# Kernel optimization log

Hardware: AMD Instinct MI355X
Metric: run time of the kernel (lower is better)

## Reference

```python
import jax, jax.numpy as jnp
import numpy as np

D_MODEL = 256; N_HEADS = 8; HEAD_DIM = 32; N_LEVELS = 4; N_POINTS = 4; N_LAYERS = 3; D_FFN = 1024
SHAPES = np.array([[76, 76], [38, 38], [19, 19], [10, 10]], dtype=np.int64)
S_TOTAL = int((SHAPES[:, 0] * SHAPES[:, 1]).sum())  # 7681


def setup_inputs():
    key = jax.random.key(0)
    ks = jax.random.split(key, 12)
    B = 1; C = D_MODEL; M = N_HEADS; Lv = N_LEVELS; P = N_POINTS; L = N_LAYERS; s = 0.02
    starts = np.concatenate([[0], np.cumsum(SHAPES[:, 0] * SHAPES[:, 1])[:-1]]).astype(np.int64)
    inp = {
        "src": jax.random.normal(ks[0], (B, S_TOTAL, C), jnp.float32),
        "pos": jax.random.normal(ks[1], (B, S_TOTAL, C), jnp.float32),
        "valid_ratios": jnp.ones((B, Lv, 2), jnp.float32),
        "spatial_shapes": jnp.asarray(SHAPES),
        "level_start_index": jnp.asarray(starts),
        "padding_mask": jnp.zeros((B, S_TOTAL), bool),
        "W_off": jax.random.normal(ks[2], (L, C, M * Lv * P * 2), jnp.float32) * s,
        "b_off": jax.random.normal(ks[3], (L, M * Lv * P * 2), jnp.float32) * s,
        "W_attn": jax.random.normal(ks[4], (L, C, M * Lv * P), jnp.float32) * s,
        "b_attn": jax.random.normal(ks[5], (L, M * Lv * P), jnp.float32) * s,
        "W_val": jax.random.normal(ks[6], (L, C, C), jnp.float32) * s,
        "b_val": jnp.zeros((L, C), jnp.float32),
        "W_out": jax.random.normal(ks[7], (L, C, C), jnp.float32) * s,
        "b_out": jnp.zeros((L, C), jnp.float32),
        "ln1_g": jnp.ones((L, C), jnp.float32),
        "ln1_b": jnp.zeros((L, C), jnp.float32),
        "W_ff1": jax.random.normal(ks[8], (L, C, D_FFN), jnp.float32) * s,
        "b_ff1": jnp.zeros((L, D_FFN), jnp.float32),
        "W_ff2": jax.random.normal(ks[9], (L, D_FFN, C), jnp.float32) * s,
        "b_ff2": jnp.zeros((L, C), jnp.float32),
        "ln2_g": jnp.ones((L, C), jnp.float32),
        "ln2_b": jnp.zeros((L, C), jnp.float32),
    }
    return inp


def _ln(x, g, b):
    mu = x.mean(-1, keepdims=True)
    var = ((x - mu) ** 2).mean(-1, keepdims=True)
    return (x - mu) * jax.lax.rsqrt(var + 1e-5) * g + b


def _gather(v, idx):
    # v: [B, HW, M, D], idx: [B, S, M, P] -> [B, S, M, P, D], head-specific gather
    B, S, M, P = idx.shape
    def one(vb, ib):
        i2 = ib.transpose(0, 2, 1).reshape(S * P, M, 1)
        o = jnp.take_along_axis(vb, i2, axis=0)  # [S*P, M, D]
        return o.reshape(S, P, M, -1).transpose(0, 2, 1, 3)
    return jax.vmap(one)(v, idx)


def _msda(query, src, mask, ref, shapes, starts, Wo, bo, Wa, ba, Wv, bv, Wout, bout):
    # Multi-scale deformable attention (Deformable-DETR), grid_sample align_corners=False + zero padding
    B, S, C = src.shape
    M, Lv, P, D = N_HEADS, N_LEVELS, N_POINTS, HEAD_DIM
    value = src @ Wv + bv
    value = jnp.where(mask[..., None], 0.0, value).reshape(B, S, M, D)
    off = (query @ Wo + bo).reshape(B, S, M, Lv, P, 2)
    aw = jax.nn.softmax((query @ Wa + ba).reshape(B, S, M, Lv * P), -1).reshape(B, S, M, Lv, P)
    norm = jnp.asarray(shapes[:, ::-1].copy(), jnp.float32)  # (W, H) per level
    loc = ref[:, :, None, :, None, :] + off / norm[None, None, None, :, None, :]  # [B,S,M,Lv,P,2]
    out = jnp.zeros((B, S, M, D), query.dtype)
    for lvl in range(Lv):
        H = int(shapes[lvl, 0]); W = int(shapes[lvl, 1]); st = int(starts[lvl])
        v = value[:, st:st + H * W]  # [B, H*W, M, D]
        l = loc[:, :, :, lvl]  # [B, S, M, P, 2]
        x = l[..., 0] * W - 0.5
        y = l[..., 1] * H - 0.5
        x0 = jnp.floor(x); y0 = jnp.floor(y)
        dx = x - x0; dy = y - y0
        samp = jnp.zeros((B, S, M, P, D), query.dtype)
        for yy, xx, w in ((y0, x0, (1 - dy) * (1 - dx)), (y0, x0 + 1, (1 - dy) * dx),
                          (y0 + 1, x0, dy * (1 - dx)), (y0 + 1, x0 + 1, dy * dx)):
            valid = (xx >= 0) & (xx < W) & (yy >= 0) & (yy < H)
            xi = jnp.clip(xx, 0, W - 1).astype(jnp.int32)
            yi = jnp.clip(yy, 0, H - 1).astype(jnp.int32)
            g = _gather(v, yi * W + xi)
            samp = samp + (w * valid)[..., None] * g
        out = out + (aw[:, :, :, lvl, :, None] * samp).sum(3)
    return out.reshape(B, S, C) @ Wout + bout


def _ref_points(vr, shapes):
    refs = []
    for lvl in range(shapes.shape[0]):
        H = int(shapes[lvl, 0]); W = int(shapes[lvl, 1])
        ry, rx = np.meshgrid(np.linspace(0.5, H - 0.5, H, dtype=np.float32),
                             np.linspace(0.5, W - 0.5, W, dtype=np.float32), indexing="ij")
        rxj = jnp.asarray(rx.reshape(-1))[None] / (vr[:, None, lvl, 0] * W)
        ryj = jnp.asarray(ry.reshape(-1))[None] / (vr[:, None, lvl, 1] * H)
        refs.append(jnp.stack([rxj, ryj], -1))
    ref = jnp.concatenate(refs, 1)  # [B, S, 2]
    return ref[:, :, None] * vr[:, None]  # [B, S, Lv, 2]


def _encoder(src, pos, valid_ratios, shapes, starts, mask, params):
    (W_off, b_off, W_attn, b_attn, W_val, b_val, W_out, b_out,
     ln1_g, ln1_b, W_ff1, b_ff1, W_ff2, b_ff2, ln2_g, ln2_b) = params
    ref = _ref_points(valid_ratios, shapes)
    out = src
    for l in range(N_LAYERS):
        q = out + pos  # with_pos_embed
        a = _msda(q, out, mask, ref, shapes, starts, W_off[l], b_off[l], W_attn[l], b_attn[l],
                  W_val[l], b_val[l], W_out[l], b_out[l])
        out = _ln(out + a, ln1_g[l], ln1_b[l])
        f = jax.nn.relu(out @ W_ff1[l] + b_ff1[l]) @ W_ff2[l] + b_ff2[l]
        out = _ln(out + f, ln2_g[l], ln2_b[l])
    return out


def reference(src, pos, valid_ratios, spatial_shapes, level_start_index, padding_mask,
              W_off, b_off, W_attn, b_attn, W_val, b_val, W_out, b_out,
              ln1_g, ln1_b, W_ff1, b_ff1, W_ff2, b_ff2, ln2_g, ln2_b):
    shapes = np.asarray(spatial_shapes)
    starts = np.asarray(level_start_index)
    params = (W_off, b_off, W_attn, b_attn, W_val, b_val, W_out, b_out,
              ln1_g, ln1_b, W_ff1, b_ff1, W_ff2, b_ff2, ln2_g, ln2_b)
    return _encoder(src, pos, valid_ratios, shapes, starts, padding_mask, params)
```

## Files before the change

### kernel.cpp

```cpp
#include <hip/hip_runtime.h>
#include <hip/hip_bf16.h>
#include <math.h>

#define S_TOTAL 7681

typedef __attribute__((ext_vector_type(8))) short bf16x8;
typedef __attribute__((ext_vector_type(4))) float f32x4;

__device__ __forceinline__ short f2b(float x) {
    union { float f; unsigned u; } v; v.f = x;
    unsigned r = v.u + 0x7FFFu + ((v.u >> 16) & 1u);
    return (short)(r >> 16);
}
__device__ __forceinline__ float b2f(unsigned short u) {
    union { unsigned u; float f; } t; t.u = ((unsigned)u) << 16; return t.f;
}

__device__ __forceinline__ void gll16(const short* g, short* l) {
    __builtin_amdgcn_global_load_lds(
        (const __attribute__((address_space(1))) unsigned int*)g,
        (__attribute__((address_space(3))) unsigned int*)l,
        16, 0, 0);
}

#define MFMA16(a, b, c) __builtin_amdgcn_mfma_f32_16x16x32_bf16(a, b, c, 0, 0, 0)

__global__ __launch_bounds__(256) void transpose_cvt_kernel(
    const float* __restrict__ s0, const float* __restrict__ s1,
    const float* __restrict__ s2, const float* __restrict__ s3,
    const float* __restrict__ s4, const float* __restrict__ s5,
    short* __restrict__ d0, short* __restrict__ d1, short* __restrict__ d2,
    short* __restrict__ d3, short* __restrict__ d4, short* __restrict__ d5)
{
    const int z = blockIdx.z;
    int t = blockIdx.x;
    const float* src; short* dst; int K, N, lt;
    if (t < 64)       { src = s0 + (size_t)z * 65536;  dst = d0 + (size_t)z * 65536;  K = 256;  N = 256;  lt = t; }
    else if (t < 128) { src = s1 + (size_t)z * 65536;  dst = d1 + (size_t)z * 98304;  K = 256;  N = 256;  lt = t - 64; }
    else if (t < 160) { src = s2 + (size_t)z * 32768;  dst = d2 + (size_t)z * 98304;  K = 256;  N = 128;  lt = t - 128; }
    else if (t < 224) { src = s3 + (size_t)z * 65536;  dst = d3 + (size_t)z * 65536;  K = 256;  N = 256;  lt = t - 160; }
    else if (t < 480) { src = s4 + (size_t)z * 262144; dst = d4 + (size_t)z * 262144; K = 256;  N = 1024; lt = t - 224; }
    else              { src = s5 + (size_t)z * 262144; dst = d5 + (size_t)z * 262144; K = 1024; N = 256;  lt = t - 480; }
    const int ntx = N >> 5;
    const int tk = (lt / ntx) << 5, tn = (lt % ntx) << 5;
    __shared__ float tile[32][33];
    const int cx = threadIdx.x & 31, cy = threadIdx.x >> 5;
    #pragma unroll
    for (int i = 0; i < 32; i += 8)
        tile[cy + i][cx] = src[(size_t)(tk + cy + i) * N + tn + cx];
    __syncthreads();
    #pragma unroll
    for (int i = 0; i < 32; i += 8)
        dst[(size_t)(tn + cy + i) * K + tk + cx] = f2b(tile[cx][cy + i]);
}

__global__ __launch_bounds__(256) void gemm_va_kernel(
    const short* __restrict__ xb, const short* __restrict__ qb,
    const short* __restrict__ Wt_val, const short* __restrict__ Wt_oa,
    const float* __restrict__ b_val, const float* __restrict__ b_off,
    const float* __restrict__ b_attn,
    short* __restrict__ value_bf, float* __restrict__ offbuf, int M)
{
    const int grp = (blockIdx.y >= 4);
    const short* A  = grp ? qb : xb;
    const short* Wt = grp ? Wt_oa : Wt_val;
    const int colBase = (grp ? (blockIdx.y - 4) : blockIdx.y) * 64;
    const int K = 256;

    __shared__ __align__(16) short As[2][128 * 32];
    __shared__ __align__(16) short Bs[2][64 * 32];

    const int tid = threadIdx.x;
    const int lane = tid & 63;
    const int wave = tid >> 6;
    const int rowBase = blockIdx.x * 128;

    const int sr  = lane >> 2;
    const int skp = (lane & 3) * 8;
    const short* gA0 = A + (size_t)min(rowBase + wave * 16 + sr, M - 1) * K + skp;
    const short* gA1 = A + (size_t)min(rowBase + 64 + wave * 16 + sr, M - 1) * K + skp;
    const short* gB  = Wt + (size_t)(colBase + wave * 16 + sr) * K + skp;

    const int frow = lane & 15;
    const int fko  = (lane >> 4) * 8;
    const int wm = wave * 32;

    f32x4 acc[2][4] = {};

    gll16(gA0, &As[0][wave * 512]);
    gll16(gA1, &As[0][2048 + wave * 512]);
    gll16(gB,  &Bs[0][wave * 512]);
    __syncthreads();

    int cur = 0;
    for (int k0 = 0; k0 < K; k0 += 32) {
        const int nxt = cur ^ 1;
        if (k0 + 32 < K) {
            gll16(gA0 + k0 + 32, &As[nxt][wave * 512]);
            gll16(gA1 + k0 + 32, &As[nxt][2048 + wave * 512]);
            gll16(gB  + k0 + 32, &Bs[nxt][wave * 512]);
        }
        bf16x8 af0 = *(const bf16x8*)&As[cur][(wm + frow) * 32 + fko];
        bf16x8 af1 = *(const bf16x8*)&As[cur][(wm + 16 + frow) * 32 + fko];
        #pragma unroll
        for (int j = 0; j < 4; ++j) {
            bf16x8 bfj = *(const bf16x8*)&Bs[cur][(j * 16 + frow) * 32 + fko];
            acc[0][j] = MFMA16(af0, bfj, acc[0][j]);
            acc[1][j] = MFMA16(af1, bfj, acc[1][j]);
        }
        __syncthreads();
        cur = nxt;
    }

    const int erow = (lane >> 4) * 4;
    const int ecol = lane & 15;
    #pragma unroll
    for (int mi = 0; mi < 2; ++mi) {
        #pragma unroll
        for (int j = 0; j < 4; ++j) {
            int col = colBase + j * 16 + ecol;
            float bias = grp ? (col < 256 ? b_off[col] : b_attn[col - 256]) : b_val[col];
            #pragma unroll
            for (int r = 0; r < 4; ++r) {
                int row = rowBase + wm + mi * 16 + erow + r;
                if (row < M) {
                    float v = acc[mi][j][r] + bias;
                    if (grp) offbuf[(size_t)row * 384 + col] = v;
                    else     value_bf[(size_t)row * 256 + col] = f2b(v);
                }
            }
        }
    }
}

template<int RELU, int OUTBF>
__global__ __launch_bounds__(256) void gemm_kernel(
    const short* __restrict__ A, const short* __restrict__ Wt,
    const float* __restrict__ bias, void* __restrict__ Cv,
    int M, int N, int K)
{
    __shared__ __align__(16) short As[2][128 * 32];
    __shared__ __align__(16) short Bs[2][64 * 32];

    const int tid = threadIdx.x;
    const int lane = tid & 63;
    const int wave = tid >> 6;
    const int rowBase = blockIdx.x * 128;
    const int colBase = blockIdx.y * 64;

    const int sr  = lane >> 2;
    const int skp = (lane & 3) * 8;
    const short* gA0 = A + (size_t)min(rowBase + wave * 16 + sr, M - 1) * K + skp;
    const short* gA1 = A + (size_t)min(rowBase + 64 + wave * 16 + sr, M - 1) * K + skp;
    const short* gB  = Wt + (size_t)(colBase + wave * 16 + sr) * K + skp;

    const int frow = lane & 15;
    const int fko  = (lane >> 4) * 8;
    const int wm = wave * 32;

    f32x4 acc[2][4] = {};

    gll16(gA0, &As[0][wave * 512]);
    gll16(gA1, &As[0][2048 + wave * 512]);
    gll16(gB,  &Bs[0][wave * 512]);
    __syncthreads();

    int cur = 0;
    for (int k0 = 0; k0 < K; k0 += 32) {
        const int nxt = cur ^ 1;
        if (k0 + 32 < K) {
            gll16(gA0 + k0 + 32, &As[nxt][wave * 512]);
            gll16(gA1 + k0 + 32, &As[nxt][2048 + wave * 512]);
            gll16(gB  + k0 + 32, &Bs[nxt][wave * 512]);
        }
        bf16x8 af0 = *(const bf16x8*)&As[cur][(wm + frow) * 32 + fko];
        bf16x8 af1 = *(const bf16x8*)&As[cur][(wm + 16 + frow) * 32 + fko];
        #pragma unroll
        for (int j = 0; j < 4; ++j) {
            bf16x8 bfj = *(const bf16x8*)&Bs[cur][(j * 16 + frow) * 32 + fko];
            acc[0][j] = MFMA16(af0, bfj, acc[0][j]);
            acc[1][j] = MFMA16(af1, bfj, acc[1][j]);
        }
        __syncthreads();
        cur = nxt;
    }

    const int erow = (lane >> 4) * 4;
    const int ecol = lane & 15;
    #pragma unroll
    for (int mi = 0; mi < 2; ++mi) {
        #pragma unroll
        for (int j = 0; j < 4; ++j) {
            #pragma unroll
            for (int r = 0; r < 4; ++r) {
                int row = rowBase + wm + mi * 16 + erow + r;
                if (row < M) {
                    int col = colBase + j * 16 + ecol;
                    float v = acc[mi][j][r] + bias[col];
                    if (RELU) v = fmaxf(v, 0.f);
                    if (OUTBF) ((short*)Cv)[(size_t)row * N + col] = f2b(v);
                    else       ((float*)Cv)[(size_t)row * N + col] = v;
                }
            }
        }
    }
}

template<int WRITEQ>
__global__ __launch_bounds__(256) void gemm_ln_kernel(
    const short* __restrict__ A, const short* __restrict__ Wt,
    const float* __restrict__ bias, const float* __restrict__ g,
    const float* __restrict__ bln, const float* __restrict__ pos,
    float* __restrict__ out, short* __restrict__ xb, short* __restrict__ qb,
    int M, int K)
{
    __shared__ __align__(16) short As[2][16 * 32];
    __shared__ __align__(16) short Bs[2][256 * 32];
    __shared__ float rsum[16][4], rsq[16][4], smu[16], srs[16];

    const int tid = threadIdx.x;
    const int lane = tid & 63;
    const int wave = tid >> 6;
    const int rowBase = blockIdx.x * 16;

    const int sr  = lane >> 2;
    const int skp = (lane & 3) * 8;
    const short* gA = A + (size_t)min(rowBase + sr, M - 1) * K + skp;
    const short* gB = Wt + (size_t)(wave * 16 + sr) * K + skp;

    const int frow = lane & 15;
    const int fko  = (lane >> 4) * 8;

    f32x4 acc[4] = {};

    if (wave == 0) gll16(gA, &As[0][0]);
    gll16(gB,                       &Bs[0][wave * 512]);
    gll16(gB + (size_t)64  * K,     &Bs[0][2048 + wave * 512]);
    gll16(gB + (size_t)128 * K,     &Bs[0][4096 + wave * 512]);
    gll16(gB + (size_t)192 * K,     &Bs[0][6144 + wave * 512]);
    __syncthreads();

    int cur = 0;
    for (int k0 = 0; k0 < K; k0 += 32) {
        const int nxt = cur ^ 1;
        if (k0 + 32 < K) {
            const int kn = k0 + 32;
            if (wave == 0) gll16(gA + kn, &As[nxt][0]);
            gll16(gB + kn,                   &Bs[nxt][wave * 512]);
            gll16(gB + (size_t)64  * K + kn, &Bs[nxt][2048 + wave * 512]);
            gll16(gB + (size_t)128 * K + kn, &Bs[nxt][4096 + wave * 512]);
            gll16(gB + (size_t)192 * K + kn, &Bs[nxt][6144 + wave * 512]);
        }
        bf16x8 af = *(const bf16x8*)&As[cur][frow * 32 + fko];
        #pragma unroll
        for (int j = 0; j < 4; ++j) {
            bf16x8 bfj = *(const bf16x8*)&Bs[cur][(wave * 64 + j * 16 + frow) * 32 + fko];
            acc[j] = MFMA16(af, bfj, acc[j]);
        }
        __syncthreads();
        cur = nxt;
    }

    const int erow = (lane >> 4) * 4;
    const int ecol = lane & 15;
    float x[4][4];
    #pragma unroll
    for (int j = 0; j < 4; ++j)
        #pragma unroll
        for (int r = 0; r < 4; ++r) {
            int row = rowBase + erow + r;
            int col = wave * 64 + j * 16 + ecol;
            float res = (row < M) ? out[(size_t)row * 256 + col] : 0.f;
            x[j][r] = acc[j][r] + bias[col] + res;
        }

    #pragma unroll
    for (int r = 0; r < 4; ++r) {
        float s1 = x[0][r] + x[1][r] + x[2][r] + x[3][r];
        float s2 = x[0][r]*x[0][r] + x[1][r]*x[1][r]
                 + x[2][r]*x[2][r] + x[3][r]*x[3][r];
        #pragma unroll
        for (int o = 1; o < 16; o <<= 1) {
            s1 += __shfl_xor(s1, o);
            s2 += __shfl_xor(s2, o);
        }
        if ((lane & 15) == 0) {
            rsum[erow + r][wave] = s1;
            rsq [erow + r][wave] = s2;
        }
    }
    __syncthreads();
    if (tid < 16) {
        float S1 = rsum[tid][0] + rsum[tid][1] + rsum[tid][2] + rsum[tid][3];
        float S2 = rsq[tid][0] + rsq[tid][1] + rsq[tid][2] + rsq[tid][3];
        float mu = S1 * (1.f / 256.f);
        smu[tid] = mu;
        srs[tid] = rsqrtf(S2 * (1.f / 256.f) - mu * mu + 1e-5f);
    }
    __syncthreads();

    #pragma unroll
    for (int r = 0; r < 4; ++r) {
        int lrow = erow + r;
        int row = rowBase + lrow;
        if (row >= M) continue;
        float mu = smu[lrow], rs = srs[lrow];
        #pragma unroll
        for (int j = 0; j < 4; ++j) {
            int col = wave * 64 + j * 16 + ecol;
            float y = (x[j][r] - mu) * rs * g[col] + bln[col];
            out[(size_t)row * 256 + col] = y;
            xb[(size_t)row * 256 + col] = f2b(y);
            if (WRITEQ)
                qb[(size_t)row * 256 + col] = f2b(y + pos[(size_t)row * 256 + col]);
        }
    }
}

__global__ __launch_bounds__(256) void msda_kernel(
    const short* __restrict__ value, const float* __restrict__ offb,
    short* __restrict__ msdab)
{
    __shared__ float   soff[8 * 384];
    __shared__ ushort4 sIdx[1024];
    __shared__ float4  sWgt[1024];

    const int bid = blockIdx.x;
    const int sb = (bid & 7) * 121 + (bid >> 3);
    const int q0 = sb * 8;
    if (q0 >= S_TOTAL) return;
    const int tid = threadIdx.x;

    {
        const float4* src4 = (const float4*)offb;
        #pragma unroll
        for (int i = tid; i < 768; i += 256) {
            int qi = i / 96, j = i - qi * 96;
            int q = min(q0 + qi, S_TOTAL - 1);
            *(float4*)&soff[qi * 384 + j * 4] = src4[(size_t)q * 96 + j];
        }
    }
    __syncthreads();

    if (tid < 64) {
        const int qi = tid >> 3, m = tid & 7;
        float* lg = &soff[qi * 384 + 256 + m * 16];
        float mx = -1e30f;
        #pragma unroll
        for (int k = 0; k < 16; ++k) mx = fmaxf(mx, lg[k]);
        float e[16], sum = 0.f;
        #pragma unroll
        for (int k = 0; k < 16; ++k) { e[k] = expf(lg[k] - mx); sum += e[k]; }
        float inv = 1.f / sum;
        #pragma unroll
        for (int k = 0; k < 16; ++k) lg[k] = e[k] * inv;
    }
    __syncthreads();

    #pragma unroll
    for (int it = tid; it < 1024; it += 256) {
        const int qi = it >> 7, i = it & 127;
        const int lvl = (i >> 2) & 3;
        const int q = min(q0 + qi, S_TOTAL - 1);

        float refx, refy;
        if (q < 5776)      { int t = q;        int r = t / 76, c = t % 76; refx = (c + 0.5f) / 76.f; refy = (r + 0.5f) / 76.f; }
        else if (q < 7220) { int t = q - 5776; int r = t / 38, c = t % 38; refx = (c + 0.5f) / 38.f; refy = (r + 0.5f) / 38.f; }
        else if (q < 7581) { int t = q - 7220; int r = t / 19, c = t % 19; refx = (c + 0.5f) / 19.f; refy = (r + 0.5f) / 19.f; }
        else               { int t = q - 7581; int r = t / 10, c = t % 10; refx = (c + 0.5f) / 10.f; refy = (r + 0.5f) / 10.f; }

        const int LVL_HW[4] = {76, 38, 19, 10};
        const int LVL_ST[4] = {0, 5776, 7220, 7581};
        const int W = LVL_HW[lvl];
        const float fW = (float)W;

        float ox = soff[qi * 384 + i * 2];
        float oy = soff[qi * 384 + i * 2 + 1];
        float aw = soff[qi * 384 + 256 + i];

        float x = refx * fW + ox - 0.5f;
        float y = refy * fW + oy - 0.5f;
        float x0f = floorf(x), y0f = floorf(y);
        int x0 = (int)x0f, y0 = (int)y0f;
        float dx = x - x0f, dy = y - y0f;

        bool vx0 = (x0 >= 0) & (x0 < W);
        bool vx1 = (x0 >= -1) & (x0 < W - 1);
        bool vy0 = (y0 >= 0) & (y0 < W);
        bool vy1 = (y0 >= -1) & (y0 < W - 1);
        int xc0 = min(max(x0, 0), W - 1), xc1 = min(max(x0 + 1, 0), W - 1);
        int yc0 = min(max(y0, 0), W - 1), yc1 = min(max(y0 + 1, 0), W - 1);
        int base = LVL_ST[lvl];
        ushort4 id;
        id.x = (unsigned short)(base + yc0 * W + xc0);
        id.y = (unsigned short)(base + yc0 * W + xc1);
        id.z = (unsigned short)(base + yc1 * W + xc0);
        id.w = (unsigned short)(base + yc1 * W + xc1);
        float4 w4;
        w4.x = (vy0 && vx0) ? (1.f - dy) * (1.f - dx) * aw : 0.f;
        w4.y = (vy0 && vx1) ? (1.f - dy) * dx * aw : 0.f;
        w4.z = (vy1 && vx0) ? dy * (1.f - dx) * aw : 0.f;
        w4.w = (vy1 && vx1) ? dy * dx * aw : 0.f;
        sIdx[it] = id;
        sWgt[it] = w4;
    }
    __syncthreads();

    const int lane = tid & 63;
    const int qi = (tid >> 6) * 2 + (lane >> 5);
    const int q = q0 + qi;
    if (q >= S_TOTAL) return;
    const int l32 = lane & 31;
    const int h = l32 >> 2, dg = l32 & 3;
    const short* vcol = value + h * 32 + dg * 8;
    const int itb = qi * 128 + (h << 4);

    float a[8] = {};
    #pragma unroll
    for (int pt = 0; pt < 16; ++pt) {
        const ushort4 id = sIdx[itb + pt];
        const float4 w = sWgt[itb + pt];
        bf16x8 v0 = *(const bf16x8*)(vcol + ((size_t)id.x << 8));
        bf16x8 v1 = *(const bf16x8*)(vcol + ((size_t)id.y << 8));
        bf16x8 v2 = *(const bf16x8*)(vcol + ((size_t)id.z << 8));
        bf16x8 v3 = *(const bf16x8*)(vcol + ((size_t)id.w << 8));
        #pragma unroll
        for (int e = 0; e < 8; ++e)
            a[e] += w.x * b2f((unsigned short)v0[e]) + w.y * b2f((unsigned short)v1[e])
                  + w.z * b2f((unsigned short)v2[e]) + w.w * b2f((unsigned short)v3[e]);
    }
    bf16x8 o;
    #pragma unroll
    for (int e = 0; e < 8; ++e) o[e] = f2b(a[e]);
    *(bf16x8*)(msdab + (size_t)q * 256 + h * 32 + dg * 8) = o;
}

__global__ __launch_bounds__(256) void cvt_copy_kernel(
    const float4* __restrict__ src, const float4* __restrict__ pos,
    float4* __restrict__ o, ushort4* __restrict__ xb, ushort4* __restrict__ qb,
    int n4)
{
    int i = blockIdx.x * blockDim.x + threadIdx.x;
    if (i < n4) {
        float4 v = src[i], p = pos[i];
        o[i] = v;
        ushort4 h, hq;
        h.x = (unsigned short)f2b(v.x); h.y = (unsigned short)f2b(v.y);
        h.z = (unsigned short)f2b(v.z); h.w = (unsigned short)f2b(v.w);
        hq.x = (unsigned short)f2b(v.x + p.x); hq.y = (unsigned short)f2b(v.y + p.y);
        hq.z = (unsigned short)f2b(v.z + p.z); hq.w = (unsigned short)f2b(v.w + p.w);
        xb[i] = h;
        qb[i] = hq;
    }
}

extern "C" void kernel_launch(void* const* d_in, const int* in_sizes, int n_in,
                              void* d_out, int out_size, void* d_ws, size_t ws_size,
                              hipStream_t stream) {
    const float* src    = (const float*)d_in[0];
    const float* pos    = (const float*)d_in[1];
    const float* W_off  = (const float*)d_in[6];
    const float* b_off  = (const float*)d_in[7];
    const float* W_attn = (const float*)d_in[8];
    const float* b_attn = (const float*)d_in[9];
    const float* W_val  = (const float*)d_in[10];
    const float* b_val  = (const float*)d_in[11];
    const float* W_out  = (const float*)d_in[12];
    const float* b_out  = (const float*)d_in[13];
    const float* ln1_g  = (const float*)d_in[14];
    const float* ln1_b  = (const float*)d_in[15];
    const float* W_ff1  = (const float*)d_in[16];
    const float* b_ff1  = (const float*)d_in[17];
    const float* W_ff2  = (const float*)d_in[18];
    const float* b_ff2  = (const float*)d_in[19];
    const float* ln2_g  = (const float*)d_in[20];
    const float* ln2_b  = (const float*)d_in[21];

    const size_t S = S_TOTAL;
    float* out = (float*)d_out;

    short* wt = (short*)d_ws;
    short* Wt_val = wt;
    short* Wt_oa  = wt + 196608;
    short* Wt_out = wt + 491520;
    short* Wt_ff1 = wt + 688128;
    short* Wt_ff2 = wt + 1474560;
    float* fbase  = (float*)d_ws + 1131648;
    short* xb       = (short*)fbase;
    short* qb       = (short*)(fbase + 128 * S);
    short* value_bf = (short*)(fbase + 256 * S);
    float* offb     = fbase + 384 * S;
    short* msdab    = (short*)(fbase + 768 * S);
    short* hid      = (short*)(fbase + 256 * S);

    transpose_cvt_kernel<<<dim3(736, 1, 3), 256, 0, stream>>>(
        W_val, W_off, W_attn, W_out, W_ff1, W_ff2,
        Wt_val, Wt_oa, Wt_oa + 65536, Wt_out, Wt_ff1, Wt_ff2);

    const int n4 = (int)(S * 256 / 4);
    const int g4 = (n4 + 255) / 256;
    cvt_copy_kernel<<<g4, 256, 0, stream>>>((const float4*)src, (const float4*)pos,
                                            (float4*)out, (ushort4*)xb, (ushort4*)qb, n4);

    const int MB = (S_TOTAL + 127) / 128;
    const int LB = (S_TOTAL + 15) / 16;

    for (int l = 0; l < 3; ++l) {
        gemm_va_kernel<<<dim3(MB, 10), 256, 0, stream>>>(
            xb, qb, Wt_val + (size_t)l * 65536, Wt_oa + (size_t)l * 98304,
            b_val + (size_t)l * 256, b_off + (size_t)l * 256, b_attn + (size_t)l * 128,
            value_bf, offb, S_TOTAL);
        msda_kernel<<<968, 256, 0, stream>>>(value_bf, offb, msdab);
        gemm_ln_kernel<0><<<LB, 256, 0, stream>>>(
            msdab, Wt_out + (size_t)l * 65536, b_out + (size_t)l * 256,
            ln1_g + (size_t)l * 256, ln1_b + (size_t)l * 256, pos,
            out, xb, qb, S_TOTAL, 256);
        gemm_kernel<1, 1><<<dim3(MB, 16), 256, 0, stream>>>(
            xb, Wt_ff1 + (size_t)l * 262144, b_ff1 + (size_t)l * 1024, hid,
            S_TOTAL, 1024, 256);
        gemm_ln_kernel<1><<<LB, 256, 0, stream>>>(
            hid, Wt_ff2 + (size_t)l * 262144, b_ff2 + (size_t)l * 256,
            ln2_g + (size_t)l * 256, ln2_b + (size_t)l * 256, pos,
            out, xb, qb, S_TOTAL, 1024);
    }
}
```

Measured before the change: 382.6 us.

## Use BK=64 with XOR-swizzled LDS tiles and fuse input conversion into weight transpose

All three bf16 GEMM kernels now stage a K-tile of 64 instead of 32, which halves the number of barrier rounds. The LDS layout is XOR-swizzled so the wider MFMA fragment reads avoid bank conflicts. The __syncthreads calls are replaced with explicit vmcnt waits plus raw s_barrier so the next tile's loads can stay in flight. Separately, the src/pos conversion kernel is merged into the weight-transpose kernel as extra blocks, removing one launch. The trade-offs are double the LDS per block, which can lower occupancy (notably in gemm_ln, with 256x64 B tiles), and hand-counted vmcnt values that must match the issued load count.

```diff
diff --git a/kernel.cpp b/kernel.cpp
--- a/kernel.cpp
+++ b/kernel.cpp
@@ -23,6 +23,8 @@
         16, 0, 0);
 }
 
+#define SBAR() asm volatile("s_barrier" ::: "memory")
+
 #define MFMA16(a, b, c) __builtin_amdgcn_mfma_f32_16x16x32_bf16(a, b, c, 0, 0, 0)
 
 __global__ __launch_bounds__(256) void transpose_cvt_kernel(
@@ -30,10 +32,28 @@
     const float* __restrict__ s2, const float* __restrict__ s3,
     const float* __restrict__ s4, const float* __restrict__ s5,
     short* __restrict__ d0, short* __restrict__ d1, short* __restrict__ d2,
-    short* __restrict__ d3, short* __restrict__ d4, short* __restrict__ d5)
+    short* __restrict__ d3, short* __restrict__ d4, short* __restrict__ d5,
+    const float4* __restrict__ csrc, const float4* __restrict__ cpos,
+    float4* __restrict__ co, ushort4* __restrict__ cxb, ushort4* __restrict__ cqb)
 {
     const int z = blockIdx.z;
     int t = blockIdx.x;
+    if (t >= 736) {
+        const int n4 = S_TOTAL * 64;
+        int i = (z * 641 + (t - 736)) * 256 + threadIdx.x;
+        if (i < n4) {
+            float4 v = csrc[i], p = cpos[i];
+            co[i] = v;
+            ushort4 h, hq;
+            h.x = (unsigned short)f2b(v.x); h.y = (unsigned short)f2b(v.y);
+            h.z = (unsigned short)f2b(v.z); h.w = (unsigned short)f2b(v.w);
+            hq.x = (unsigned short)f2b(v.x + p.x); hq.y = (unsigned short)f2b(v.y + p.y);
+            hq.z = (unsigned short)f2b(v.z + p.z); hq.w = (unsigned short)f2b(v.w + p.w);
+            cxb[i] = h;
+            cqb[i] = hq;
+        }
+        return;
+    }
     const float* src; short* dst; int K, N, lt;
     if (t < 64)       { src = s0 + (size_t)z * 65536;  dst = d0 + (size_t)z * 65536;  K = 256;  N = 256;  lt = t; }
     else if (t < 128) { src = s1 + (size_t)z * 65536;  dst = d1 + (size_t)z * 98304;  K = 256;  N = 256;  lt = t - 64; }
@@ -53,6 +73,7 @@
     for (int i = 0; i < 32; i += 8)
         dst[(size_t)(tn + cy + i) * K + tk + cx] = f2b(tile[cx][cy + i]);
 }
+
 
 __global__ __launch_bounds__(256) void gemm_va_kernel(
     const short* __restrict__ xb, const short* __restrict__ qb,
@@ -67,49 +88,67 @@
     const int colBase = (grp ? (blockIdx.y - 4) : blockIdx.y) * 64;
     const int K = 256;
 
-    __shared__ __align__(16) short As[2][128 * 32];
-    __shared__ __align__(16) short Bs[2][64 * 32];
+    __shared__ __align__(16) short As[2][128 * 64];
+    __shared__ __align__(16) short Bs[2][64 * 64];
 
     const int tid = threadIdx.x;
     const int lane = tid & 63;
     const int wave = tid >> 6;
     const int rowBase = blockIdx.x * 128;
 
-    const int sr  = lane >> 2;
-    const int skp = (lane & 3) * 8;
-    const short* gA0 = A + (size_t)min(rowBase + wave * 16 + sr, M - 1) * K + skp;
-    const short* gA1 = A + (size_t)min(rowBase + 64 + wave * 16 + sr, M - 1) * K + skp;
-    const short* gB  = Wt + (size_t)(colBase + wave * 16 + sr) * K + skp;
+    const int sr = lane >> 3;
+    const int sc = ((lane & 7) ^ sr) << 3;
+
+    const short* gA[4];
+    #pragma unroll
+    for (int c = 0; c < 4; ++c)
+        gA[c] = A + (size_t)min(rowBase + wave * 32 + c * 8 + sr, M - 1) * K + sc;
+    const short* gB[2];
+    #pragma unroll
+    for (int c = 0; c < 2; ++c)
+        gB[c] = Wt + (size_t)(colBase + wave * 16 + c * 8 + sr) * K + sc;
 
     const int frow = lane & 15;
-    const int fko  = (lane >> 4) * 8;
+    const int g4 = lane >> 4;
+    const int r7 = frow & 7;
     const int wm = wave * 32;
 
     f32x4 acc[2][4] = {};
 
-    gll16(gA0, &As[0][wave * 512]);
-    gll16(gA1, &As[0][2048 + wave * 512]);
-    gll16(gB,  &Bs[0][wave * 512]);
-    __syncthreads();
+    auto stage = [&](int buf, int k0) {
+        #pragma unroll
+        for (int c = 0; c < 4; ++c)
+            gll16(gA[c] + k0, &As[buf][(wave * 32 + c * 8) * 64]);
+        #pragma unroll
+        for (int c = 0; c < 2; ++c)
+            gll16(gB[c] + k0, &Bs[buf][(wave * 16 + c * 8) * 64]);
+    };
+
+    stage(0, 0);
 
     int cur = 0;
-    for (int k0 = 0; k0 < K; k0 += 32) {
-        const int nxt = cur ^ 1;
-        if (k0 + 32 < K) {
-            gll16(gA0 + k0 + 32, &As[nxt][wave * 512]);
-            gll16(gA1 + k0 + 32, &As[nxt][2048 + wave * 512]);
-            gll16(gB  + k0 + 32, &Bs[nxt][wave * 512]);
-        }
-        bf16x8 af0 = *(const bf16x8*)&As[cur][(wm + frow) * 32 + fko];
-        bf16x8 af1 = *(const bf16x8*)&As[cur][(wm + 16 + frow) * 32 + fko];
-        #pragma unroll
-        for (int j = 0; j < 4; ++j) {
-            bf16x8 bfj = *(const bf16x8*)&Bs[cur][(j * 16 + frow) * 32 + fko];
-            acc[0][j] = MFMA16(af0, bfj, acc[0][j]);
-            acc[1][j] = MFMA16(af1, bfj, acc[1][j]);
-        }
-        __syncthreads();
-        cur = nxt;
+    for (int k0 = 0; k0 < K; k0 += 64) {
+        if (k0 + 64 < K) {
+            stage(cur ^ 1, k0 + 64);
+            asm volatile("s_waitcnt vmcnt(6)" ::: "memory");
+        } else {
+            asm volatile("s_waitcnt vmcnt(0)" ::: "memory");
+        }
+        SBAR();
+        #pragma unroll
+        for (int kk8 = 0; kk8 < 8; kk8 += 4) {
+            const int ua = (((kk8 + g4) ^ r7) << 3);
+            bf16x8 af0 = *(const bf16x8*)&As[cur][(wm + frow) * 64 + ua];
+            bf16x8 af1 = *(const bf16x8*)&As[cur][(wm + 16 + frow) * 64 + ua];
+            #pragma unroll
+            for (int j = 0; j < 4; ++j) {
+                bf16x8 bfj = *(const bf16x8*)&Bs[cur][(j * 16 + frow) * 64 + ua];
+                acc[0][j] = MFMA16(af0, bfj, acc[0][j]);
+                acc[1][j] = MFMA16(af1, bfj, acc[1][j]);
+            }
+        }
+        SBAR();
+        cur ^= 1;
     }
 
     const int erow = (lane >> 4) * 4;
@@ -139,8 +178,8 @@
     const float* __restrict__ bias, void* __restrict__ Cv,
     int M, int N, int K)
 {
-    __shared__ __align__(16) short As[2][128 * 32];
-    __shared__ __align__(16) short Bs[2][64 * 32];
+    __shared__ __align__(16) short As[2][128 * 64];
+    __shared__ __align__(16) short Bs[2][64 * 64];
 
     const int tid = threadIdx.x;
     const int lane = tid & 63;
@@ -148,41 +187,59 @@
     const int rowBase = blockIdx.x * 128;
     const int colBase = blockIdx.y * 64;
 
-    const int sr  = lane >> 2;
-    const int skp = (lane & 3) * 8;
-    const short* gA0 = A + (size_t)min(rowBase + wave * 16 + sr, M - 1) * K + skp;
-    const short* gA1 = A + (size_t)min(rowBase + 64 + wave * 16 + sr, M - 1) * K + skp;
-    const short* gB  = Wt + (size_t)(colBase + wave * 16 + sr) * K + skp;
+    const int sr = lane >> 3;
+    const int sc = ((lane & 7) ^ sr) << 3;
+
+    const short* gA[4];
+    #pragma unroll
+    for (int c = 0; c < 4; ++c)
+        gA[c] = A + (size_t)min(rowBase + wave * 32 + c * 8 + sr, M - 1) * K + sc;
+    const short* gB[2];
+    #pragma unroll
+    for (int c = 0; c < 2; ++c)
+        gB[c] = Wt + (size_t)(colBase + wave * 16 + c * 8 + sr) * K + sc;
 
     const int frow = lane & 15;
-    const int fko  = (lane >> 4) * 8;
+    const int g4 = lane >> 4;
+    const int r7 = frow & 7;
     const int wm = wave * 32;
 
     f32x4 acc[2][4] = {};
 
-    gll16(gA0, &As[0][wave * 512]);
-    gll16(gA1, &As[0][2048 + wave * 512]);
-    gll16(gB,  &Bs[0][wave * 512]);
-    __syncthreads();
+    auto stage = [&](int buf, int k0) {
+        #pragma unroll
+        for (int c = 0; c < 4; ++c)
+            gll16(gA[c] + k0, &As[buf][(wave * 32 + c * 8) * 64]);
+        #pragma unroll
+        for (int c = 0; c < 2; ++c)
+            gll16(gB[c] + k0, &Bs[buf][(wave * 16 + c * 8) * 64]);
+    };
+
+    stage(0, 0);
 
     int cur = 0;
-    for (int k0 = 0; k0 < K; k0 += 32) {
-        const int nxt = cur ^ 1;
-        if (k0 + 32 < K) {
-            gll16(gA0 + k0 + 32, &As[nxt][wave * 512]);
-            gll16(gA1 + k0 + 32, &As[nxt][2048 + wave * 512]);
-            gll16(gB  + k0 + 32, &Bs[nxt][wave * 512]);
-        }
-        bf16x8 af0 = *(const bf16x8*)&As[cur][(wm + frow) * 32 + fko];
-        bf16x8 af1 = *(const bf16x8*)&As[cur][(wm + 16 + frow) * 32 + fko];
-        #pragma unroll
-        for (int j = 0; j < 4; ++j) {
-            bf16x8 bfj = *(const bf16x8*)&Bs[cur][(j * 16 + frow) * 32 + fko];
-            acc[0][j] = MFMA16(af0, bfj, acc[0][j]);
-            acc[1][j] = MFMA16(af1, bfj, acc[1][j]);
-        }
-        __syncthreads();
-        cur = nxt;
+    for (int k0 = 0; k0 < K; k0 += 64) {
+        if (k0 + 64 < K) {
+            stage(cur ^ 1, k0 + 64);
+            asm volatile("s_waitcnt vmcnt(6)" ::: "memory");
+        } else {
+            asm volatile("s_waitcnt vmcnt(0)" ::: "memory");
+        }
+        SBAR();
+        #pragma unroll
+        for (int kk8 = 0; kk8 < 8; kk8 += 4) {
+            const int ua = (((kk8 + g4) ^ r7) << 3);
+            bf16x8 af0 = *(const bf16x8*)&As[cur][(wm + frow) * 64 + ua];
+            bf16x8 af1 = *(const bf16x8*)&As[cur][(wm + 16 + frow) * 64 + ua];
+            #pragma unroll
+            for (int j = 0; j < 4; ++j) {
+                bf16x8 bfj = *(const bf16x8*)&Bs[cur][(j * 16 + frow) * 64 + ua];
+                acc[0][j] = MFMA16(af0, bfj, acc[0][j]);
+                acc[1][j] = MFMA16(af1, bfj, acc[1][j]);
+            }
+        }
+        SBAR();
+        cur ^= 1;
     }
 
     const int erow = (lane >> 4) * 4;
@@ -214,8 +271,8 @@
     float* __restrict__ out, short* __restrict__ xb, short* __restrict__ qb,
     int M, int K)
 {
-    __shared__ __align__(16) short As[2][16 * 32];
-    __shared__ __align__(16) short Bs[2][256 * 32];
+    __shared__ __align__(16) short As[2][16 * 64];
+    __shared__ __align__(16) short Bs[2][256 * 64];
     __shared__ float rsum[16][4], rsq[16][4], smu[16], srs[16];
 
     const int tid = threadIdx.x;
@@ -223,42 +280,52 @@
     const int wave = tid >> 6;
     const int rowBase = blockIdx.x * 16;
 
-    const int sr  = lane >> 2;
-    const int skp = (lane & 3) * 8;
-    const short* gA = A + (size_t)min(rowBase + sr, M - 1) * K + skp;
-    const short* gB = Wt + (size_t)(wave * 16 + sr) * K + skp;
+    const int sr = lane >> 3;
+    const int sc = ((lane & 7) ^ sr) << 3;
+
+    const short* gA = A + (size_t)min(rowBase + wave * 8 + sr, M - 1) * K + sc;
+    const short* gB[8];
+    #pragma unroll
+    for (int c = 0; c < 8; ++c)
+        gB[c] = Wt + (size_t)(wave * 64 + c * 8 + sr) * K + sc;
 
     const int frow = lane & 15;
-    const int fko  = (lane >> 4) * 8;
+    const int g4 = lane >> 4;
+    const int r7 = frow & 7;
 
     f32x4 acc[4] = {};
 
-    if (wave == 0) gll16(gA, &As[0][0]);
-    gll16(gB,                       &Bs[0][wave * 512]);
-    gll16(gB + (size_t)64  * K,     &Bs[0][2048 + wave * 512]);
-    gll16(gB + (size_t)128 * K,     &Bs[0][4096 + wave * 512]);
-    gll16(gB + (size_t)192 * K,     &Bs[0][6144 + wave * 512]);
-    __syncthreads();
+    auto stage = [&](int buf, int k0) {
+        if (wave < 2) gll16(gA + k0, &As[buf][(wave * 8) * 64]);
+        #pragma unroll
+        for (int c = 0; c < 8; ++c)
+            gll16(gB[c] + k0, &Bs[buf][(wave * 64 + c * 8) * 64]);
+    };
+
+    stage(0, 0);
 
     int cur = 0;
-    for (int k0 = 0; k0 < K; k0 += 32) {
-        const int nxt = cur ^ 1;
-        if (k0 + 32 < K) {
-            const int kn = k0 + 32;
-            if (wave == 0) gll16(gA + kn, &As[nxt][0]);
-            gll16(gB + kn,                   &Bs[nxt][wave * 512]);
-            gll16(gB + (size_t)64  * K + kn, &Bs[nxt][2048 + wave * 512]);
-            gll16(gB + (size_t)128 * K + kn, &Bs[nxt][4096 + wave * 512]);
-            gll16(gB + (size_t)192 * K + kn, &Bs[nxt][6144 + wave * 512]);
-        }
-        bf16x8 af = *(const bf16x8*)&As[cur][frow * 32 + fko];
-        #pragma unroll
-        for (int j = 0; j < 4; ++j) {
-            bf16x8 bfj = *(const bf16x8*)&Bs[cur][(wave * 64 + j * 16 + frow) * 32 + fko];
-            acc[j] = MFMA16(af, bfj, acc[j]);
-        }
-        __syncthreads();
-        cur = nxt;
+    for (int k0 = 0; k0 < K; k0 += 64) {
+        if (k0 + 64 < K) {
+            stage(cur ^ 1, k0 + 64);
+            if (wave < 2) asm volatile("s_waitcnt vmcnt(9)" ::: "memory");
+            else          asm volatile("s_waitcnt vmcnt(8)" ::: "memory");
+        } else {
+            asm volatile("s_waitcnt vmcnt(0)" ::: "memory");
+        }
+        SBAR();
+        #pragma unroll
+        for (int kk8 = 0; kk8 < 8; kk8 += 4) {
+            const int ua = (((kk8 + g4) ^ r7) << 3);
+            bf16x8 af = *(const bf16x8*)&As[cur][frow * 64 + ua];
+            #pragma unroll
+            for (int j = 0; j < 4; ++j) {
+                bf16x8 bfj = *(const bf16x8*)&Bs[cur][(wave * 64 + j * 16 + frow) * 64 + ua];
+                acc[j] = MFMA16(af, bfj, acc[j]);
+            }
+        }
+        SBAR();
+        cur ^= 1;
     }
 
     const int erow = (lane >> 4) * 4;
@@ -433,25 +500,6 @@
     #pragma unroll
     for (int e = 0; e < 8; ++e) o[e] = f2b(a[e]);
     *(bf16x8*)(msdab + (size_t)q * 256 + h * 32 + dg * 8) = o;
-}
-
-__global__ __launch_bounds__(256) void cvt_copy_kernel(
-    const float4* __restrict__ src, const float4* __restrict__ pos,
-    float4* __restrict__ o, ushort4* __restrict__ xb, ushort4* __restrict__ qb,
-    int n4)
-{
-    int i = blockIdx.x * blockDim.x + threadIdx.x;
-    if (i < n4) {
-        float4 v = src[i], p = pos[i];
-        o[i] = v;
-        ushort4 h, hq;
-        h.x = (unsigned short)f2b(v.x); h.y = (unsigned short)f2b(v.y);
-        h.z = (unsigned short)f2b(v.z); h.w = (unsigned short)f2b(v.w);
-        hq.x = (unsigned short)f2b(v.x + p.x); hq.y = (unsigned short)f2b(v.y + p.y);
-        hq.z = (unsigned short)f2b(v.z + p.z); hq.w = (unsigned short)f2b(v.w + p.w);
-        xb[i] = h;
-        qb[i] = hq;
-    }
 }
 
 extern "C" void kernel_launch(void* const* d_in, const int* in_sizes, int n_in,
@@ -493,14 +541,11 @@
     short* msdab    = (short*)(fbase + 768 * S);
     short* hid      = (short*)(fbase + 256 * S);
 
-    transpose_cvt_kernel<<<dim3(736, 1, 3), 256, 0, stream>>>(
+    transpose_cvt_kernel<<<dim3(1377, 1, 3), 256, 0, stream>>>(
         W_val, W_off, W_attn, W_out, W_ff1, W_ff2,
-        Wt_val, Wt_oa, Wt_oa + 65536, Wt_out, Wt_ff1, Wt_ff2);
-
-    const int n4 = (int)(S * 256 / 4);
-    const int g4 = (n4 + 255) / 256;
-    cvt_copy_kernel<<<g4, 256, 0, stream>>>((const float4*)src, (const float4*)pos,
-                                            (float4*)out, (ushort4*)xb, (ushort4*)qb, n4);
+        Wt_val, Wt_oa, Wt_oa + 65536, Wt_out, Wt_ff1, Wt_ff2,
+        (const float4*)src, (const float4*)pos,
+        (float4*)out, (ushort4*)xb, (ushort4*)qb);
 
     const int MB = (S_TOTAL + 127) / 128;
     const int LB = (S_TOTAL + 15) / 16;
```

Result: faster. 367.5 us (-3.9%).
